# Kernel tuning notes

Hardware: AMD Instinct MI355X
Metric: run time of the kernel (lower is better)

Reference implementation:

```python
import jax, jax.numpy as jnp
import numpy as np

NUM_HEADS = 16
WINDOW = 16  # hard-coded in module; half-window = 8


def sliding_mask(seq_len):
    # mask[i, j] = 0 if j in [i - W//2, i + W//2], else -inf  (additive)
    i = jnp.arange(seq_len)[:, None]
    j = jnp.arange(seq_len)[None, :]
    return jnp.where(jnp.abs(i - j) <= WINDOW // 2, 0.0, -jnp.inf).astype(jnp.float32)


def setup_inputs() -> dict:
    key = jax.random.key(0)
    k1, k2, k3 = jax.random.split(key, 3)
    B, S, D = 2, 2048, 1024
    scale = 1.0 / np.sqrt(D)
    return {
        "input_embeddings": jax.random.normal(k1, (B, S, D), dtype=jnp.float32),
        "token_ids": jax.random.randint(k2, (B, S), 0, 32000, dtype=jnp.int64),
        # nn.MultiheadAttention params: packed in_proj [3D, D] + bias, out_proj [D, D] + bias
        "w_qkv": jax.random.normal(jax.random.fold_in(k3, 0), (3 * D, D), dtype=jnp.float32) * scale,
        "b_qkv": jnp.zeros((3 * D,), dtype=jnp.float32),
        "w_out": jax.random.normal(jax.random.fold_in(k3, 1), (D, D), dtype=jnp.float32) * scale,
        "b_out": jnp.zeros((D,), dtype=jnp.float32),
    }


def reference(input_embeddings, token_ids, w_qkv, b_qkv, w_out, b_out):
    B, S, D = input_embeddings.shape
    H = NUM_HEADS
    hd = D // H
    # packed QKV projection (torch in_proj): [B, S, 3D]
    qkv = input_embeddings @ w_qkv.T + b_qkv
    q, k, v = jnp.split(qkv, 3, axis=-1)
    # [B, H, S, hd]
    q = q.reshape(B, S, H, hd).transpose(0, 2, 1, 3)
    k = k.reshape(B, S, H, hd).transpose(0, 2, 1, 3)
    v = v.reshape(B, S, H, hd).transpose(0, 2, 1, 3)
    scores = jnp.einsum("bhqd,bhkd->bhqk", q, k) / jnp.sqrt(jnp.asarray(hd, q.dtype))
    scores = scores + sliding_mask(S)  # broadcast additive [S, S] mask
    attn = jax.nn.softmax(scores, axis=-1)
    ctx = jnp.einsum("bhqk,bhkd->bhqd", attn, v)
    ctx = ctx.transpose(0, 2, 1, 3).reshape(B, S, D)
    return ctx @ w_out.T + b_out
```

## Files before the change

kernel.cpp:

```cpp
#include <hip/hip_runtime.h>
#include <stdint.h>


typedef __bf16 bf16_t;
typedef bf16_t bf16x8 __attribute__((ext_vector_type(8)));
typedef unsigned short u16x8 __attribute__((ext_vector_type(8)));
typedef float f32x4 __attribute__((ext_vector_type(4)));

#define GLD16(g, l)                                                        \
  __builtin_amdgcn_global_load_lds(                                        \
      (const __attribute__((address_space(1))) void*)(g),                  \
      (__attribute__((address_space(3))) void*)(l), 16, 0, 0)

__device__ __forceinline__ unsigned short f2bf(float f) {
  unsigned int u = __float_as_uint(f);
  u += 0x7FFFu + ((u >> 16) & 1u);
  return (unsigned short)(u >> 16);
}

__device__ __forceinline__ bf16x8 ld16(const unsigned short* p) {
  return __builtin_bit_cast(bf16x8, *reinterpret_cast<const u16x8*>(p));
}

__global__ void cvt_all(const float* __restrict__ x, const float* __restrict__ wq,
                        const float* __restrict__ wo, unsigned short* __restrict__ xb,
                        unsigned short* __restrict__ wqb,
                        unsigned short* __restrict__ wob) {
  const int N0 = 1048576, N1 = 786432, N2 = 262144;
  for (int i = blockIdx.x * blockDim.x + threadIdx.x; i < N0 + N1 + N2;
       i += gridDim.x * blockDim.x) {
    const float4* src;
    unsigned short* dst;
    int j;
    if (i < N0) { src = (const float4*)x; dst = xb; j = i; }
    else if (i < N0 + N1) { src = (const float4*)wq; dst = wqb; j = i - N0; }
    else { src = (const float4*)wo; dst = wob; j = i - N0 - N1; }
    const float4 f = src[j];
    ushort4 o;
    o.x = f2bf(f.x); o.y = f2bf(f.y); o.z = f2bf(f.z); o.w = f2bf(f.w);
    reinterpret_cast<ushort4*>(dst)[j] = o;
  }
}

template <int EPI>
__global__ __launch_bounds__(256, 2) void gemm_bt(
    const unsigned short* __restrict__ A,
    const unsigned short* __restrict__ Bt,
    const float* __restrict__ bias,
    unsigned short* __restrict__ Cq, unsigned short* __restrict__ Ck,
    unsigned short* __restrict__ Cv, float* __restrict__ Cp, int M, int N,
    int K) {
  __shared__ unsigned short sA[128 * 64];
  __shared__ unsigned short sB[128 * 64];

  const int tid = threadIdx.x;
  const int wave = tid >> 6;
  const int lane = tid & 63;
  const int m0 = blockIdx.x * 128;
  const int n0 = blockIdx.y * 128;
  const int wr = wave >> 1;
  const int wc = wave & 1;

  f32x4 acc[4][4] = {};

  const int srow = (wave << 3) + (lane >> 3);
  const int sslot = ((lane & 7) ^ (lane >> 3)) << 3;
  const unsigned short* Ag = A + (size_t)(m0 + srow) * K + sslot;
  const unsigned short* Bg = Bt + (size_t)(n0 + srow) * K + sslot;
  const int wdst = wave * 512;

  const int kg = lane >> 4;
  const int l7 = lane & 7;

  for (int k0 = 0; k0 < K; k0 += 64) {
    __syncthreads();
#pragma unroll
    for (int r = 0; r < 4; ++r) {
      GLD16(Ag + (size_t)(r * 32) * K + k0, &sA[r * 2048 + wdst]);
      GLD16(Bg + (size_t)(r * 32) * K + k0, &sB[r * 2048 + wdst]);
    }
    __syncthreads();

    bf16x8 af[2][4], bfr[2][4];
#pragma unroll
    for (int st = 0; st < 2; ++st) {
#pragma unroll
      for (int f = 0; f < 4; ++f) {
        const int ar = wr * 64 + f * 16 + (lane & 15);
        const int br = wc * 64 + f * 16 + (lane & 15);
        const int se = ((st << 2) | kg) ^ l7;
        af[st][f] = ld16(&sA[ar * 64 + (se << 3)]);
        bfr[st][f] = ld16(&sB[br * 64 + (se << 3)]);
      }
    }
#pragma unroll
    for (int st = 0; st < 2; ++st)
#pragma unroll
      for (int i = 0; i < 4; ++i)
#pragma unroll
        for (int j = 0; j < 4; ++j)
          acc[i][j] = __builtin_amdgcn_mfma_f32_16x16x32_bf16(
              af[st][i], bfr[st][j], acc[i][j], 0, 0, 0);
  }

#pragma unroll
  for (int i = 0; i < 4; ++i) {
    const int row0 = m0 + wr * 64 + i * 16 + ((lane >> 4) << 2);
#pragma unroll
    for (int j = 0; j < 4; ++j) {
      const int col = n0 + wc * 64 + j * 16 + (lane & 15);
      const float bb = bias[col];
#pragma unroll
      for (int r = 0; r < 4; ++r) {
        const int m = row0 + r;
        const float val = acc[i][j][r] + bb;
        if (EPI == 0) {
          Cp[(size_t)m * N + col] = val;
        } else {
          const int b = m >> 11, s = m & 2047;
          const int which = col >> 10, nn = col & 1023;
          const int h = nn >> 6, d = nn & 63;
          const int bh = (b << 4) + h;
          const unsigned short vb = f2bf(val);
          if (which == 0)
            Cq[((size_t)(bh * 2048 + s)) * 64 + d] = vb;
          else if (which == 1)
            Ck[((size_t)(bh * 2048 + s)) * 64 + d] = vb;
          else
            Cv[((size_t)(bh * 64 + d)) * 2048 + s] = vb;
        }
      }
    }
  }
}

__global__ __launch_bounds__(256) void attn_mfma(
    const unsigned short* __restrict__ Qb, const unsigned short* __restrict__ Kb,
    const unsigned short* __restrict__ Vt, unsigned short* __restrict__ ctx) {
  __shared__ unsigned short P[4][16][40];
  const int wave = threadIdx.x >> 6;
  const int lane = threadIdx.x & 63;
  const int gw = (blockIdx.x << 2) + wave;
  const int bh = gw >> 7;
  const int i0 = (gw & 127) << 4;
  const int qr = lane & 15;
  const int kg = lane >> 4;
  const int kc = kg << 3;

  const size_t qbase = ((size_t)(bh * 2048 + i0 + qr)) * 64;
  const bf16x8 aq0 = ld16(Qb + qbase + kc);
  const bf16x8 aq1 = ld16(Qb + qbase + 32 + kc);

  f32x4 sc0 = {0.f, 0.f, 0.f, 0.f}, sc1 = {0.f, 0.f, 0.f, 0.f};
  {
    const int ka0 = i0 - 8 + qr;
    const int ka1 = ka0 + 16;
    const int kcl0 = min(max(ka0, 0), 2047);
    const int kcl1 = min(max(ka1, 0), 2047);
    const unsigned short* K0 = Kb + ((size_t)(bh * 2048 + kcl0)) * 64;
    const unsigned short* K1 = Kb + ((size_t)(bh * 2048 + kcl1)) * 64;
    sc0 = __builtin_amdgcn_mfma_f32_16x16x32_bf16(aq0, ld16(K0 + kc), sc0, 0, 0, 0);
    sc0 = __builtin_amdgcn_mfma_f32_16x16x32_bf16(aq1, ld16(K0 + 32 + kc), sc0, 0, 0, 0);
    sc1 = __builtin_amdgcn_mfma_f32_16x16x32_bf16(aq0, ld16(K1 + kc), sc1, 0, 0, 0);
    sc1 = __builtin_amdgcn_mfma_f32_16x16x32_bf16(aq1, ld16(K1 + 32 + kc), sc1, 0, 0, 0);
  }

  unsigned short* Pw = &P[wave][0][0];
  float lsum[4];
#pragma unroll
  for (int r = 0; r < 4; ++r) {
    const int q = (kg << 2) + r;
    const int key0 = qr, key1 = 16 + qr;
    const int ka0 = i0 - 8 + key0, ka1 = i0 - 8 + key1;
    const bool v0 = (q <= key0) && (key0 <= q + 16) && (ka0 >= 0) && (ka0 < 2048);
    const bool v1 = (q <= key1) && (key1 <= q + 16) && (ka1 >= 0) && (ka1 < 2048);
    const float e0 = v0 ? __expf(sc0[r] * 0.125f) : 0.f;
    const float e1 = v1 ? __expf(sc1[r] * 0.125f) : 0.f;
    Pw[q * 40 + key0] = f2bf(e0);
    Pw[q * 40 + key1] = f2bf(e1);
    float s = e0 + e1;
#pragma unroll
    for (int off = 1; off < 16; off <<= 1) s += __shfl_xor(s, off);
    lsum[r] = s;
  }

  const bf16x8 pa = ld16(&Pw[qr * 40 + kc]);

  const int base_s = min(max(i0 - 8 + kc, 0), 2040);
  f32x4 o[4];
  const f32x4 zero = {0.f, 0.f, 0.f, 0.f};
#pragma unroll
  for (int t2 = 0; t2 < 4; ++t2) {
    const unsigned short* Vr =
        Vt + ((size_t)(bh * 64 + t2 * 16 + qr)) * 2048 + base_s;
    o[t2] = __builtin_amdgcn_mfma_f32_16x16x32_bf16(pa, ld16(Vr), zero, 0, 0, 0);
  }

  const int b = bh >> 4, h = bh & 15;
  float rinv[4];
#pragma unroll
  for (int r = 0; r < 4; ++r) rinv[r] = 1.0f / lsum[r];
#pragma unroll
  for (int t2 = 0; t2 < 4; ++t2) {
#pragma unroll
    for (int r = 0; r < 4; ++r) {
      const int q = (kg << 2) + r;
      const int d = t2 * 16 + qr;
      ctx[((size_t)(b * 2048 + i0 + q)) * 1024 + (h << 6) + d] =
          f2bf(o[t2][r] * rinv[r]);
    }
  }
}

extern "C" void kernel_launch(void* const* d_in, const int* in_sizes, int n_in,
                              void* d_out, int out_size, void* d_ws,
                              size_t ws_size, hipStream_t stream) {
  const float* x = (const float*)d_in[0];
  const float* w_qkv = (const float*)d_in[2];
  const float* b_qkv = (const float*)d_in[3];
  const float* w_out = (const float*)d_in[4];
  const float* b_out = (const float*)d_in[5];
  float* out = (float*)d_out;

  char* ws = (char*)d_ws;
  unsigned short* xb    = (unsigned short*)(ws + 0);
  unsigned short* wqkvb = (unsigned short*)(ws + 8388608);
  unsigned short* woutb = (unsigned short*)(ws + 14680064);
  unsigned short* Qb    = (unsigned short*)(ws + 16777216);
  unsigned short* Kb    = (unsigned short*)(ws + 25165824);
  unsigned short* Vt    = (unsigned short*)(ws + 33554432);
  unsigned short* ctxb  = (unsigned short*)(ws + 41943040);

  cvt_all<<<2048, 256, 0, stream>>>(x, w_qkv, w_out, xb, wqkvb, woutb);

  gemm_bt<1><<<dim3(32, 24), 256, 0, stream>>>(xb, wqkvb, b_qkv, Qb, Kb, Vt,
                                               nullptr, 4096, 3072, 1024);

  attn_mfma<<<1024, 256, 0, stream>>>(Qb, Kb, Vt, ctxb);

  gemm_bt<0><<<dim3(32, 8), 256, 0, stream>>>(ctxb, woutb, b_out, nullptr,
                                              nullptr, nullptr, out, 4096,
                                              1024, 1024);
}
```

Baseline: 80.40 us.

## Double-buffer GEMM shared-memory tiles with async global-to-LDS prefetch two stages ahead

The GEMM main loop now uses two LDS buffers for the A and B tiles and issues the global_load_lds copies for tile t+2 while tile t is being computed. Hand-placed vmcnt/lgkmcnt waits and raw barriers replace the two __syncthreads per iteration. The aim is to hide global memory latency behind the MFMA work. LDS usage per block doubles to 64 KB, which may limit occupancy at 2 blocks per CU, and correctness depends on the hand-counted vmcnt value.

```diff
diff --git a/kernel.cpp b/kernel.cpp
--- a/kernel.cpp
+++ b/kernel.cpp
@@ -50,8 +50,8 @@
     unsigned short* __restrict__ Cq, unsigned short* __restrict__ Ck,
     unsigned short* __restrict__ Cv, float* __restrict__ Cp, int M, int N,
     int K) {
-  __shared__ unsigned short sA[128 * 64];
-  __shared__ unsigned short sB[128 * 64];
+  __shared__ unsigned short sA[2][8192];
+  __shared__ unsigned short sB[2][8192];
 
   const int tid = threadIdx.x;
   const int wave = tid >> 6;
@@ -69,30 +69,50 @@
   const unsigned short* Bg = Bt + (size_t)(n0 + srow) * K + sslot;
   const int wdst = wave * 512;
 
+  const int T = K >> 6;
+
+  auto stage = [&](int t, int b) {
+#pragma unroll
+    for (int r = 0; r < 4; ++r) {
+      GLD16(Ag + (size_t)(r * 32) * K + t * 64, &sA[b][r * 2048 + wdst]);
+      GLD16(Bg + (size_t)(r * 32) * K + t * 64, &sB[b][r * 2048 + wdst]);
+    }
+  };
+
+  stage(0, 0);
+  stage(1, 1);
+
   const int kg = lane >> 4;
   const int l7 = lane & 7;
-
-  for (int k0 = 0; k0 < K; k0 += 64) {
-    __syncthreads();
-#pragma unroll
-    for (int r = 0; r < 4; ++r) {
-      GLD16(Ag + (size_t)(r * 32) * K + k0, &sA[r * 2048 + wdst]);
-      GLD16(Bg + (size_t)(r * 32) * K + k0, &sB[r * 2048 + wdst]);
-    }
-    __syncthreads();
-
+  const int arr = wr * 64 + (lane & 15);
+  const int brr = wc * 64 + (lane & 15);
+
+  for (int t = 0; t < T; ++t) {
+    if (t < T - 1)
+      asm volatile("s_waitcnt vmcnt(8)" ::: "memory");
+    else
+      asm volatile("s_waitcnt vmcnt(0)" ::: "memory");
+    __builtin_amdgcn_s_barrier();
+
+    const int b = t & 1;
+    const unsigned short* sAb = sA[b];
+    const unsigned short* sBb = sB[b];
     bf16x8 af[2][4], bfr[2][4];
 #pragma unroll
     for (int st = 0; st < 2; ++st) {
 #pragma unroll
       for (int f = 0; f < 4; ++f) {
-        const int ar = wr * 64 + f * 16 + (lane & 15);
-        const int br = wc * 64 + f * 16 + (lane & 15);
         const int se = ((st << 2) | kg) ^ l7;
-        af[st][f] = ld16(&sA[ar * 64 + (se << 3)]);
-        bfr[st][f] = ld16(&sB[br * 64 + (se << 3)]);
+        af[st][f] = ld16(&sAb[(arr + f * 16) * 64 + (se << 3)]);
+        bfr[st][f] = ld16(&sBb[(brr + f * 16) * 64 + (se << 3)]);
       }
     }
+    asm volatile("s_waitcnt lgkmcnt(0)" ::: "memory");
+    __builtin_amdgcn_sched_barrier(0);
+    __builtin_amdgcn_s_barrier();
+
+    if (t + 2 < T) stage(t + 2, b);
+
 #pragma unroll
     for (int st = 0; st < 2; ++st)
 #pragma unroll
@@ -117,10 +137,10 @@
         if (EPI == 0) {
           Cp[(size_t)m * N + col] = val;
         } else {
-          const int b = m >> 11, s = m & 2047;
+          const int b2 = m >> 11, s = m & 2047;
           const int which = col >> 10, nn = col & 1023;
           const int h = nn >> 6, d = nn & 63;
-          const int bh = (b << 4) + h;
+          const int bh = (b2 << 4) + h;
           const unsigned short vb = f2bf(val);
           if (which == 0)
             Cq[((size_t)(bh * 2048 + s)) * 64 + d] = vb;
```

Result: no change. 79.73 us (-0.8%).
